# Optimization experiments

Hardware: AMD Instinct MI355X
Metric: run time of the kernel (lower is better)

## Reference

```python
import jax, jax.numpy as jnp
import numpy as np

NUM_HEADS = 16

def setup_inputs() -> dict:
    key = jax.random.key(0)
    ks = jax.random.split(key, 3)
    B, S, D = 2, 2048, 1024
    x = jax.random.normal(ks[0], (B, S, D), dtype=jnp.float32)
    # xavier-uniform style scaling for weights
    Wqkv = jax.random.normal(ks[1], (3 * D, D), dtype=jnp.float32) * (1.0 / jnp.sqrt(D))
    bqkv = jnp.zeros((3 * D,), dtype=jnp.float32)
    Wo = jax.random.normal(ks[2], (D, D), dtype=jnp.float32) * (1.0 / jnp.sqrt(D))
    bo = jnp.zeros((D,), dtype=jnp.float32)
    return {"x": x, "Wqkv": Wqkv, "bqkv": bqkv, "Wo": Wo, "bo": bo}

def reference(x, Wqkv, bqkv, Wo, bo):
    B, S, D = x.shape
    H = NUM_HEADS
    hd = D // H
    # qkv projection (torch Linear: x @ W.T + b)
    qkv = x @ Wqkv.T + bqkv                      # [B, S, 3D]
    qkv = qkv.reshape(B, S, H, 3 * hd).transpose(0, 2, 1, 3)  # [B, H, S, 3hd]
    q, k, v = jnp.split(qkv, 3, axis=-1)         # each [B, H, S, hd]
    scale = 1.0 / jnp.sqrt(jnp.asarray(hd, dtype=x.dtype))
    logits = jnp.einsum('bhqd,bhkd->bhqk', q, k) * scale  # [B, H, S, S]
    attn = jax.nn.softmax(logits, axis=-1)
    vals = jnp.einsum('bhqk,bhkd->bhqd', attn, v)         # [B, H, S, hd]
    vals = vals.transpose(0, 2, 1, 3).reshape(B, S, D)
    return vals @ Wo.T + bo
```

## Files before the change

kernel.cpp:

```cpp
#include <hip/hip_runtime.h>


typedef short short8 __attribute__((ext_vector_type(8)));
typedef unsigned short ushort8v __attribute__((ext_vector_type(8)));
typedef unsigned short ushort4v __attribute__((ext_vector_type(4)));
typedef float floatx4 __attribute__((ext_vector_type(4)));

#define S_LEN 2048
#define D_MODEL 1024
#define N_HEADS 16
#define HEAD_DIM 64

#define EXP2F(x) __builtin_amdgcn_exp2f(x)

__device__ inline float bf2f(unsigned int u16) {
    union { unsigned int i; float f; } v; v.i = u16 << 16; return v.f;
}
__device__ inline unsigned short f2b(float f) {
    union { float f; unsigned int u; } v; v.f = f;
    return (unsigned short)((v.u + 0x7FFFu + ((v.u >> 16) & 1u)) >> 16);
}
__device__ inline unsigned int fbits(float f) {
    union { float f; unsigned int u; } v; v.f = f; return v.u;
}
__device__ inline unsigned int pack_bf2(float lo, float hi) {
    return __byte_perm(fbits(lo) + 0x8000u, fbits(hi) + 0x8000u, 0x7632);
}

__device__ inline int key128(int c) {
    return (c & 0x63) | ((c & 0x0C) << 1) | ((c & 0x10) >> 2);
}

__device__ inline void gld_lds16(const unsigned short* g, unsigned short* lds) {
    __builtin_amdgcn_global_load_lds(
        (const __attribute__((address_space(1))) void*)g,
        (__attribute__((address_space(3))) void*)lds, 16, 0, 0);
}

__global__ __launch_bounds__(256)
void cvt3(const float* __restrict__ s0, const float* __restrict__ s1,
          const float* __restrict__ s2,
          unsigned short* __restrict__ d0, unsigned short* __restrict__ d1,
          unsigned short* __restrict__ d2,
          int n0, int n1, int n2) {
    const int total = n0 + n1 + n2;
    for (int g = blockIdx.x * blockDim.x + threadIdx.x; g < total;
         g += gridDim.x * blockDim.x) {
        const float* s; unsigned short* d; int l;
        if (g < n0)            { s = s0; d = d0; l = g; }
        else if (g < n0 + n1)  { s = s1; d = d1; l = g - n0; }
        else                   { s = s2; d = d2; l = g - n0 - n1; }
        const float4* sp = (const float4*)s + (size_t)l * 2;
        float4 f0 = sp[0], f1 = sp[1];
        ushort8v o;
        o[0] = f2b(f0.x); o[1] = f2b(f0.y); o[2] = f2b(f0.z); o[3] = f2b(f0.w);
        o[4] = f2b(f1.x); o[5] = f2b(f1.y); o[6] = f2b(f1.z); o[7] = f2b(f1.w);
        *(ushort8v*)(d + (size_t)l * 8) = o;
    }
}

__device__ inline void stage_u(const unsigned short* __restrict__ g, int ldk,
                               unsigned short* lds, int wave, int lane) {
    const int lr  = lane >> 3;
    const int csw = ((lane & 7) ^ lr) * 8;
    gld_lds16(g + (size_t)(wave * 8 + lr) * ldk + csw, lds + wave * 512);
}

#define STAGE_A(kk0, buf) do {                                                 \
    _Pragma("unroll")                                                          \
    for (int u = 0; u < 4; ++u)                                                \
        stage_u(Abase + (size_t)(u * 64) * K + (kk0), K,                       \
                &AS[buf][u * 4096], wave, lane);                               \
} while (0)
#define STAGE_B2(kk0, buf) do {                                 \
    stage_u(Bbase + (kk0),                    K, &BS[buf][0],    wave, lane);  \
    stage_u(Bbase + (size_t)64 * K + (kk0),   K, &BS[buf][4096], wave, lane);  \
} while (0)
#define STAGE_B1(kk0, buf) do {                                    \
    stage_u(Bbase + (size_t)128 * K + (kk0),  K, &BS[buf][8192], wave, lane);  \
} while (0)

#define QLDB(pBx) do {                                                         \
    _Pragma("unroll")                                                          \
    for (int nj = 0; nj < 3; ++nj) {                                           \
        bF[nj][0] = *(const short8*)((pBx) + nj * 1024 + co0);                 \
        bF[nj][1] = *(const short8*)((pBx) + nj * 1024 + co1);                 \
    }                                                                          \
} while (0)

#define QPHASE(pAx, mq, ...) do {                                              \
    short8 aF[2][2];                                                           \
    _Pragma("unroll")                                                          \
    for (int m2 = 0; m2 < 2; ++m2) {                                           \
        aF[m2][0] = *(const short8*)((pAx) + ((mq) * 2 + m2) * 1024 + co0);    \
        aF[m2][1] = *(const short8*)((pAx) + ((mq) * 2 + m2) * 1024 + co1);    \
    }                                                                          \
    __VA_ARGS__;                                                               \
    __builtin_amdgcn_s_barrier();                                              \
    __builtin_amdgcn_s_setprio(1);                                             \
    _Pragma("unroll")                                                          \
    for (int kk = 0; kk < 2; ++kk)                                             \
        _Pragma("unroll")                                                      \
        for (int m2 = 0; m2 < 2; ++m2)                                         \
            _Pragma("unroll")                                                  \
            for (int nj = 0; nj < 3; ++nj)                                     \
                acc[(mq) * 2 + m2][nj] = __builtin_amdgcn_mfma_f32_16x16x32_bf16( \
                    aF[m2][kk], bF[nj][kk], acc[(mq) * 2 + m2][nj], 0, 0, 0);  \
    __builtin_amdgcn_s_setprio(0);                                             \
    __builtin_amdgcn_s_barrier();                                              \
} while (0)

#define WAIT_VM3() asm volatile("s_waitcnt vmcnt(3)" ::: "memory")
#define WAIT_VM0() asm volatile("s_waitcnt vmcnt(0)" ::: "memory")

__global__ __launch_bounds__(512, 2)
void qkv_gemm(const unsigned short* __restrict__ x,
              const unsigned short* __restrict__ Wqkv,
              const float* __restrict__ bqkv,
              unsigned short* __restrict__ Qb,
              unsigned short* __restrict__ Kb,
              unsigned short* __restrict__ Vb) {
    __shared__ unsigned short AS[2][16384];
    __shared__ unsigned short BS[2][12288];

    const int tid  = threadIdx.x;
    const int lane = tid & 63;
    const int wave = tid >> 6;
    const int wm = wave >> 2;
    const int wn = wave & 3;
    const int r  = lane & 15, q2 = lane >> 4;
    const int K  = D_MODEL;

    const int idx = blockIdx.x;
    const int swz = (idx & 7) * 32 + (idx >> 3);
    const int mb = swz & 15, nb = swz >> 4;
    const int m0 = mb * 256, n0 = nb * 192;

    const unsigned short* Abase = x    + (size_t)m0 * K;
    const unsigned short* Bbase = Wqkv + (size_t)n0 * K;

    const int co0 = ((q2 ^ (r & 7)) * 8);
    const int co1 = (((q2 + 4) ^ (r & 7)) * 8);
    const unsigned short* pA0 = &AS[0][(wm * 128 + r) * 64];
    const unsigned short* pA1 = &AS[1][(wm * 128 + r) * 64];
    const unsigned short* pB0 = &BS[0][(wn * 48 + r) * 64];
    const unsigned short* pB1 = &BS[1][(wn * 48 + r) * 64];

    floatx4 acc[8][3] = {};
    short8 bF[3][2];

    STAGE_A(0, 0);
    STAGE_B2(0, 0); STAGE_B1(0, 0);
    STAGE_B2(64, 1); STAGE_B1(64, 1);
    WAIT_VM3();
    __builtin_amdgcn_s_barrier();

    for (int i = 0; i < 8; ++i) {
        const bool more = (i < 7);
        const int kA1 = i * 128 + 64;
        const int kT2 = i * 128 + 128;
        const int kT3 = i * 128 + 192;

        QLDB(pB0);
        QPHASE(pA0, 0, { STAGE_A(kA1, 1); });
        QPHASE(pA0, 1, { if (more) STAGE_B2(kT2, 0); });
        QPHASE(pA0, 2, { if (more) STAGE_B1(kT2, 0); });
        QPHASE(pA0, 3, {
            if (more) { WAIT_VM3(); } else { WAIT_VM0(); }
        });
        QLDB(pB1);
        QPHASE(pA1, 0, { if (more) STAGE_A(kT2, 0); });
        QPHASE(pA1, 1, { if (more) STAGE_B2(kT3, 1); });
        QPHASE(pA1, 2, { if (more) STAGE_B1(kT3, 1); });
        QPHASE(pA1, 3, {
            if (more) { WAIT_VM3(); }
        });
    }

#pragma unroll
    for (int mi = 0; mi < 8; mi++) {
#pragma unroll
        for (int nj = 0; nj < 3; nj++) {
            int rem = wn * 48 + nj * 16 + r;
            int n = n0 + rem;
            int typ = rem >> 6;
            int d = rem & 63;
            float bv = bqkv[n];
            int m = m0 + wm * 128 + mi * 16 + q2 * 4;
            int b = m >> 11, s = m & 2047;
            if (typ == 2) {
                ushort4v pk;
#pragma unroll
                for (int rg = 0; rg < 4; rg++) pk[rg] = f2b(acc[mi][nj][rg] + bv);
                *(ushort4v*)(Vb + ((size_t)((b * N_HEADS + nb) * HEAD_DIM + d)) * S_LEN + s) = pk;
            } else {
                unsigned short* dst = (typ == 0) ? Qb : Kb;
                float sc = (typ == 0) ? 0.180336880f : 1.0f;
#pragma unroll
                for (int rg = 0; rg < 4; rg++)
                    dst[(((size_t)(b * N_HEADS + nb)) * S_LEN + s + rg) * HEAD_DIM + d] =
                        f2b((acc[mi][nj][rg] + bv) * sc);
            }
        }
    }
}

__global__ __launch_bounds__(256)
void out_gemm(const unsigned short* __restrict__ vals,
              const unsigned short* __restrict__ Wo,
              const float* __restrict__ bo,
              float* __restrict__ out) {
    __shared__ unsigned short As[2][8192];
    __shared__ unsigned short Bs[2][4096];

    const int tid  = threadIdx.x;
    const int lane = tid & 63;
    const int wave = tid >> 6;
    const int wm = wave >> 1, wn = wave & 1;
    const int r = lane & 15, q2 = lane >> 4;
    const int K = D_MODEL;
    const int m0 = blockIdx.y * 128;
    const int n0 = blockIdx.x * 64;

    const unsigned short* Abase = vals + (size_t)m0 * K;
    const unsigned short* Bbase = Wo   + (size_t)n0 * K;

    const int lr  = lane >> 3;
    const int csw = ((lane & 7) ^ lr) * 8;
    const int co0 = ((q2 ^ (r & 7)) * 8);
    const int co1 = (((q2 + 4) ^ (r & 7)) * 8);

    floatx4 acc[4][2] = {};

#define OSTAGE(k0, abuf, bbuf) do {                                            \
    _Pragma("unroll")                                                          \
    for (int u = 0; u < 4; ++u)                                                \
        gld_lds16(Abase + (size_t)(u * 32 + wave * 8 + lr) * K + (k0) + csw,   \
                  (abuf) + u * 2048 + wave * 512);                             \
    _Pragma("unroll")                                                          \
    for (int u = 0; u < 2; ++u)                                                \
        gld_lds16(Bbase + (size_t)(u * 32 + wave * 8 + lr) * K + (k0) + csw,   \
                  (bbuf) + u * 2048 + wave * 512);                             \
} while (0)

    OSTAGE(0, &As[0][0], &Bs[0][0]);
    __builtin_amdgcn_s_waitcnt(0);
    __syncthreads();

    int buf = 0;
    for (int k0 = 0; k0 < K; k0 += 64) {
        const bool more = (k0 + 64 < K);
        if (more) {
            OSTAGE(k0 + 64, &As[buf ^ 1][0], &Bs[buf ^ 1][0]);
        }
#pragma unroll
        for (int kk = 0; kk < 2; kk++) {
            const int co = kk ? co1 : co0;
            short8 aF[4], bF[2];
#pragma unroll
            for (int t = 0; t < 4; t++)
                aF[t] = *(const short8*)(&As[buf][(wm * 64 + t * 16 + r) * 64] + co);
#pragma unroll
            for (int t = 0; t < 2; t++)
                bF[t] = *(const short8*)(&Bs[buf][(wn * 32 + t * 16 + r) * 64] + co);
#pragma unroll
            for (int i = 0; i < 4; i++)
#pragma unroll
                for (int j = 0; j < 2; j++)
                    acc[i][j] = __builtin_amdgcn_mfma_f32_16x16x32_bf16(aF[i], bF[j], acc[i][j], 0, 0, 0);
        }
        if (more) {
            __builtin_amdgcn_s_waitcnt(0);
            __syncthreads();
            buf ^= 1;
        }
    }
#undef OSTAGE

#pragma unroll
    for (int i = 0; i < 4; i++) {
#pragma unroll
        for (int j = 0; j < 2; j++) {
            int n = n0 + wn * 32 + j * 16 + r;
            float bv = bo[n];
#pragma unroll
            for (int rg = 0; rg < 4; rg++) {
                int m = m0 + wm * 64 + i * 16 + q2 * 4 + rg;
                out[(size_t)m * D_MODEL + n] = acc[i][j][rg] + bv;
            }
        }
    }
}

__global__ __launch_bounds__(256, 2)
void attn_kernel(const unsigned short* __restrict__ Qb,
                 const unsigned short* __restrict__ Kb,
                 const unsigned short* __restrict__ Vg,
                 unsigned short* __restrict__ vals) {
    __shared__ unsigned short Ks[2 * 128 * 64];
    __shared__ unsigned short Vts[2 * 128 * 64];

    const int tid = threadIdx.x;
    const int lane = tid & 63;
    const int wave = tid >> 6;
    const int r = lane & 15, q2 = lane >> 4;
    const int r7 = r & 7;
    const int w32 = wave * 32;

    const int idx  = blockIdx.x;
    const int xcd  = idx & 7;
    const int slot = idx >> 3;
    const int bh   = (xcd << 2) | (slot >> 4);
    const int q0   = (slot & 15) * 128;
    const int b = bh >> 4, h = bh & 15;

    const unsigned short* Qp = Qb + (size_t)bh * S_LEN * HEAD_DIM;
    const unsigned short* Kp = Kb + (size_t)bh * S_LEN * HEAD_DIM;
    const unsigned short* Vp = Vg + (size_t)bh * HEAD_DIM * S_LEN;

    const int srow = lane >> 3;
    const int scol = ((lane & 7) ^ srow) * 8;

    int krow[4], vd[4], vpan[4];
#pragma unroll
    for (int t = 0; t < 4; t++) {
        int c = wave * 32 + t * 8 + srow;
        krow[t] = key128(c);
        vpan[t] = c >> 6;
        vd[t]   = c & 63;
    }

    {
        const int qrow = tid >> 1;
        const int c0 = (tid & 1) * 4;
#pragma unroll
        for (int cc = 0; cc < 4; cc++) {
            int cb = c0 + cc;
            const uint4* gq = (const uint4*)(Qp + (size_t)(q0 + qrow) * HEAD_DIM + cb * 8);
            *(uint4*)(Ks + qrow * 64 + ((cb ^ (qrow & 7)) * 8)) = *gq;
        }
    }
    __syncthreads();
    short8 qf[2][2];
#pragma unroll
    for (int nt = 0; nt < 2; nt++)
#pragma unroll
        for (int ks = 0; ks < 2; ks++) {
            int cb = ks * 4 + q2;
            qf[nt][ks] = *(const short8*)(Ks + (w32 + nt * 16 + r) * 64 + ((cb ^ r7) * 8));
        }
    __syncthreads();

#pragma unroll
    for (int t = 0; t < 4; t++) {
        gld_lds16(Kp + (size_t)krow[t] * HEAD_DIM + scol,
                  Ks + (wave * 32 + t * 8) * 64);
        gld_lds16(Vp + (size_t)vd[t] * S_LEN + vpan[t] * 64 + scol,
                  Vts + (wave * 32 + t * 8) * 64);
    }
    __builtin_amdgcn_s_waitcnt(0);
    __syncthreads();

    union { unsigned int u[4]; short8 s; } onesu;
    onesu.u[0] = 0x3F803F80u; onesu.u[1] = 0x3F803F80u;
    onesu.u[2] = 0x3F803F80u; onesu.u[3] = 0x3F803F80u;
    const short8 onesf = onesu.s;

    floatx4 l_acc[2] = {};
    floatx4 o_acc[2][4] = {};
    int cur = 0;

    for (int kt = 0; kt < S_LEN; kt += 128) {
        const int more = (kt + 128 < S_LEN);
        if (more) {
            const int nxt = (cur ^ 1) * 8192;
#pragma unroll
            for (int t = 0; t < 4; t++) {
                gld_lds16(Kp + (size_t)(kt + 128 + krow[t]) * HEAD_DIM + scol,
                          Ks + nxt + (wave * 32 + t * 8) * 64);
                gld_lds16(Vp + (size_t)vd[t] * S_LEN + kt + 128 + vpan[t] * 64 + scol,
                          Vts + nxt + (wave * 32 + t * 8) * 64);
            }
        }
        const int co = cur * 8192;

        floatx4 sp[8][2] = {};
        __builtin_amdgcn_s_setprio(1);
#pragma unroll
        for (int mt = 0; mt < 8; mt++)
#pragma unroll
            for (int ks = 0; ks < 2; ks++) {
                int cb = ks * 4 + q2;
                short8 kfr = *(const short8*)(Ks + co + (mt * 16 + r) * 64 + ((cb ^ r7) * 8));
#pragma unroll
                for (int nt = 0; nt < 2; nt++)
                    sp[mt][nt] = __builtin_amdgcn_mfma_f32_16x16x32_bf16(kfr, qf[nt][ks], sp[mt][nt], 0, 0, 0);
            }
        __builtin_amdgcn_s_setprio(0);

#pragma unroll
        for (int nt = 0; nt < 2; nt++)
#pragma unroll
            for (int mt = 0; mt < 8; mt++)
#pragma unroll
                for (int reg = 0; reg < 4; reg++)
                    sp[mt][nt][reg] = EXP2F(sp[mt][nt][reg]);

        short8 pa[2][4];
#pragma unroll
        for (int nt = 0; nt < 2; nt++)
#pragma unroll
            for (int ks = 0; ks < 4; ks++) {
                union { unsigned int u[4]; short8 s; } tw;
                tw.u[0] = pack_bf2(sp[2 * ks][nt][0],     sp[2 * ks][nt][1]);
                tw.u[1] = pack_bf2(sp[2 * ks][nt][2],     sp[2 * ks][nt][3]);
                tw.u[2] = pack_bf2(sp[2 * ks + 1][nt][0], sp[2 * ks + 1][nt][1]);
                tw.u[3] = pack_bf2(sp[2 * ks + 1][nt][2], sp[2 * ks + 1][nt][3]);
                pa[nt][ks] = tw.s;
            }

        __builtin_amdgcn_s_setprio(1);
#pragma unroll
        for (int dt = 0; dt < 4; dt++) {
            short8 vf[4];
#pragma unroll
            for (int ks = 0; ks < 4; ks++) {
                int cb = (ks & 1) * 4 + q2;
                vf[ks] = *(const short8*)(Vts + co + (ks >> 1) * 4096 + (dt * 16 + r) * 64 + ((cb ^ r7) * 8));
            }
#pragma unroll
            for (int nt = 0; nt < 2; nt++)
#pragma unroll
                for (int ks = 0; ks < 4; ks++)
                    o_acc[nt][dt] = __builtin_amdgcn_mfma_f32_16x16x32_bf16(pa[nt][ks], vf[ks], o_acc[nt][dt], 0, 0, 0);
        }
#pragma unroll
        for (int nt = 0; nt < 2; nt++)
#pragma unroll
            for (int ks = 0; ks < 4; ks++)
                l_acc[nt] = __builtin_amdgcn_mfma_f32_16x16x32_bf16(pa[nt][ks], onesf, l_acc[nt], 0, 0, 0);
        __builtin_amdgcn_s_setprio(0);

        if (more) {
            __builtin_amdgcn_s_waitcnt(0);
            __syncthreads();
            cur ^= 1;
        }
    }

#pragma unroll
    for (int nt = 0; nt < 2; nt++) {
#pragma unroll
        for (int reg = 0; reg < 4; reg++) {
            float inv = 1.0f / l_acc[nt][reg];
            int srow2 = q0 + w32 + nt * 16 + q2 * 4 + reg;
            size_t base = ((size_t)b * S_LEN + srow2) * D_MODEL + h * HEAD_DIM + r;
#pragma unroll
            for (int dt = 0; dt < 4; dt++)
                vals[base + dt * 16] = f2b(o_acc[nt][dt][reg] * inv);
        }
    }
}

extern "C" void kernel_launch(void* const* d_in, const int* in_sizes, int n_in,
                              void* d_out, int out_size, void* d_ws, size_t ws_size,
                              hipStream_t stream) {
    const float* x    = (const float*)d_in[0];
    const float* Wqkv = (const float*)d_in[1];
    const float* bqkv = (const float*)d_in[2];
    const float* Wo   = (const float*)d_in[3];
    const float* bo   = (const float*)d_in[4];
    float* out = (float*)d_out;

    const size_t NX = 4194304, NW = 3145728, NO = 1048576;
    unsigned short* xb    = (unsigned short*)d_ws;
    unsigned short* Wqkvb = xb + NX;
    unsigned short* Wob   = Wqkvb + NW;
    unsigned short* Qb    = Wob + NO;
    unsigned short* Kb    = Qb + NX;
    unsigned short* Vb    = Kb + NX;
    unsigned short* vals  = xb;

    cvt3<<<4096, 256, 0, stream>>>(x, Wqkv, Wo, xb, Wqkvb, Wob,
                                   (int)(NX / 8), (int)(NW / 8), (int)(NO / 8));
    qkv_gemm<<<256, 512, 0, stream>>>(xb, Wqkvb, bqkv, Qb, Kb, Vb);
    attn_kernel<<<512, 256, 0, stream>>>(Qb, Kb, Vb, vals);
    out_gemm<<<dim3(16, 32), 256, 0, stream>>>(vals, Wob, bo, out);
}
```

Baseline: 174.4 us.

## Software-pipeline attention loop: overlap next QK^T with current PV, triple-buffer V

Restructures the attention inner loop so each iteration computes QK^T for tile t+1 while doing PV for tile t, with the exp/pack done after both. V moves to a three-slot LDS ring and two tiles are prefetched in the prologue, so loads run two tiles ahead. The aim is to hide exp latency and the load/barrier stalls behind MFMA work. The cost is more LDS (larger V buffer, possibly lower occupancy) and higher register pressure from keeping the packed probabilities live across the QK step.

```diff
diff --git a/kernel.cpp b/kernel.cpp
--- a/kernel.cpp
+++ b/kernel.cpp
@@ -298,7 +298,7 @@
                  const unsigned short* __restrict__ Vg,
                  unsigned short* __restrict__ vals) {
     __shared__ unsigned short Ks[2 * 128 * 64];
-    __shared__ unsigned short Vts[2 * 128 * 64];
+    __shared__ unsigned short V3[3 * 128 * 64];
 
     const int tid = threadIdx.x;
     const int lane = tid & 63;
@@ -356,9 +356,16 @@
         gld_lds16(Kp + (size_t)krow[t] * HEAD_DIM + scol,
                   Ks + (wave * 32 + t * 8) * 64);
         gld_lds16(Vp + (size_t)vd[t] * S_LEN + vpan[t] * 64 + scol,
-                  Vts + (wave * 32 + t * 8) * 64);
-    }
-    __builtin_amdgcn_s_waitcnt(0);
+                  V3 + (wave * 32 + t * 8) * 64);
+    }
+#pragma unroll
+    for (int t = 0; t < 4; t++) {
+        gld_lds16(Kp + (size_t)(128 + krow[t]) * HEAD_DIM + scol,
+                  Ks + 8192 + (wave * 32 + t * 8) * 64);
+        gld_lds16(Vp + (size_t)vd[t] * S_LEN + 128 + vpan[t] * 64 + scol,
+                  V3 + 8192 + (wave * 32 + t * 8) * 64);
+    }
+    asm volatile("s_waitcnt vmcnt(8)" ::: "memory");
     __syncthreads();
 
     union { unsigned int u[4]; short8 s; } onesu;
@@ -368,85 +375,112 @@
 
     floatx4 l_acc[2] = {};
     floatx4 o_acc[2][4] = {};
-    int cur = 0;
-
-    for (int kt = 0; kt < S_LEN; kt += 128) {
-        const int more = (kt + 128 < S_LEN);
-        if (more) {
-            const int nxt = (cur ^ 1) * 8192;
-#pragma unroll
-            for (int t = 0; t < 4; t++) {
-                gld_lds16(Kp + (size_t)(kt + 128 + krow[t]) * HEAD_DIM + scol,
-                          Ks + nxt + (wave * 32 + t * 8) * 64);
-                gld_lds16(Vp + (size_t)vd[t] * S_LEN + kt + 128 + vpan[t] * 64 + scol,
-                          Vts + nxt + (wave * 32 + t * 8) * 64);
+    floatx4 sp[8][2];
+    short8 paA[2][4];
+
+#define AZERO() do {                                                           \
+    _Pragma("unroll")                                                          \
+    for (int mt = 0; mt < 8; mt++)                                             \
+        _Pragma("unroll")                                                      \
+        for (int nt = 0; nt < 2; nt++)                                         \
+            sp[mt][nt] = (floatx4){0.f, 0.f, 0.f, 0.f};                        \
+} while (0)
+
+#define AQK(KBASE) do {                                                        \
+    _Pragma("unroll")                                                          \
+    for (int mt = 0; mt < 8; mt++)                                             \
+        _Pragma("unroll")                                                      \
+        for (int ks = 0; ks < 2; ks++) {                                       \
+            int cb = ks * 4 + q2;                                              \
+            short8 kfr = *(const short8*)(Ks + (KBASE) + (mt * 16 + r) * 64 + ((cb ^ r7) * 8)); \
+            _Pragma("unroll")                                                  \
+            for (int nt = 0; nt < 2; nt++)                                     \
+                sp[mt][nt] = __builtin_amdgcn_mfma_f32_16x16x32_bf16(kfr, qf[nt][ks], sp[mt][nt], 0, 0, 0); \
+        }                                                                      \
+} while (0)
+
+#define AEXPPACK() do {                                                        \
+    _Pragma("unroll")                                                          \
+    for (int nt = 0; nt < 2; nt++)                                             \
+        _Pragma("unroll")                                                      \
+        for (int mt = 0; mt < 8; mt++)                                         \
+            _Pragma("unroll")                                                  \
+            for (int reg = 0; reg < 4; reg++)                                  \
+                sp[mt][nt][reg] = EXP2F(sp[mt][nt][reg]);                      \
+    _Pragma("unroll")                                                          \
+    for (int nt = 0; nt < 2; nt++)                                             \
+        _Pragma("unroll")                                                      \
+        for (int ks = 0; ks < 4; ks++) {                                       \
+            union { unsigned int u[4]; short8 s; } tw;                         \
+            tw.u[0] = pack_bf2(sp[2 * ks][nt][0],     sp[2 * ks][nt][1]);      \
+            tw.u[1] = pack_bf2(sp[2 * ks][nt][2],     sp[2 * ks][nt][3]);      \
+            tw.u[2] = pack_bf2(sp[2 * ks + 1][nt][0], sp[2 * ks + 1][nt][1]);  \
+            tw.u[3] = pack_bf2(sp[2 * ks + 1][nt][2], sp[2 * ks + 1][nt][3]);  \
+            paA[nt][ks] = tw.s;                                                \
+        }                                                                      \
+} while (0)
+
+#define APVL(VBASE) do {                                                       \
+    _Pragma("unroll")                                                          \
+    for (int dt = 0; dt < 4; dt++) {                                           \
+        short8 vf[4];                                                          \
+        _Pragma("unroll")                                                      \
+        for (int ks = 0; ks < 4; ks++) {                                       \
+            int cb = (ks & 1) * 4 + q2;                                        \
+            vf[ks] = *(const short8*)(V3 + (VBASE) + (ks >> 1) * 4096 + (dt * 16 + r) * 64 + ((cb ^ r7) * 8)); \
+        }                                                                      \
+        _Pragma("unroll")                                                      \
+        for (int nt = 0; nt < 2; nt++)                                         \
+            _Pragma("unroll")                                                  \
+            for (int ks = 0; ks < 4; ks++)                                     \
+                o_acc[nt][dt] = __builtin_amdgcn_mfma_f32_16x16x32_bf16(paA[nt][ks], vf[ks], o_acc[nt][dt], 0, 0, 0); \
+    }                                                                          \
+    _Pragma("unroll")                                                          \
+    for (int nt = 0; nt < 2; nt++)                                             \
+        _Pragma("unroll")                                                      \
+        for (int ks = 0; ks < 4; ks++)                                         \
+            l_acc[nt] = __builtin_amdgcn_mfma_f32_16x16x32_bf16(paA[nt][ks], onesf, l_acc[nt], 0, 0, 0); \
+} while (0)
+
+    AZERO();
+    __builtin_amdgcn_s_setprio(1);
+    AQK(0);
+    __builtin_amdgcn_s_setprio(0);
+    AEXPPACK();
+
+    for (int t = 0; t < 15; ++t) {
+        asm volatile("s_waitcnt vmcnt(0)" ::: "memory");
+        __syncthreads();
+        if (t < 14) {
+            const int kb  = (t & 1) * 8192;
+            const int vs  = ((t + 2) % 3) * 8192;
+            const int kt2 = (t + 2) * 128;
+#pragma unroll
+            for (int tt = 0; tt < 4; tt++) {
+                gld_lds16(Kp + (size_t)(kt2 + krow[tt]) * HEAD_DIM + scol,
+                          Ks + kb + (wave * 32 + tt * 8) * 64);
+                gld_lds16(Vp + (size_t)vd[tt] * S_LEN + kt2 + vpan[tt] * 64 + scol,
+                          V3 + vs + (wave * 32 + tt * 8) * 64);
             }
         }
-        const int co = cur * 8192;
-
-        floatx4 sp[8][2] = {};
+        const int kc = ((t + 1) & 1) * 8192;
+        const int vb = (t % 3) * 8192;
+        AZERO();
         __builtin_amdgcn_s_setprio(1);
-#pragma unroll
-        for (int mt = 0; mt < 8; mt++)
-#pragma unroll
-            for (int ks = 0; ks < 2; ks++) {
-                int cb = ks * 4 + q2;
-                short8 kfr = *(const short8*)(Ks + co + (mt * 16 + r) * 64 + ((cb ^ r7) * 8));
-#pragma unroll
-                for (int nt = 0; nt < 2; nt++)
-                    sp[mt][nt] = __builtin_amdgcn_mfma_f32_16x16x32_bf16(kfr, qf[nt][ks], sp[mt][nt], 0, 0, 0);
-            }
+        AQK(kc);
+        APVL(vb);
         __builtin_amdgcn_s_setprio(0);
-
-#pragma unroll
-        for (int nt = 0; nt < 2; nt++)
-#pragma unroll
-            for (int mt = 0; mt < 8; mt++)
-#pragma unroll
-                for (int reg = 0; reg < 4; reg++)
-                    sp[mt][nt][reg] = EXP2F(sp[mt][nt][reg]);
-
-        short8 pa[2][4];
-#pragma unroll
-        for (int nt = 0; nt < 2; nt++)
-#pragma unroll
-            for (int ks = 0; ks < 4; ks++) {
-                union { unsigned int u[4]; short8 s; } tw;
-                tw.u[0] = pack_bf2(sp[2 * ks][nt][0],     sp[2 * ks][nt][1]);
-                tw.u[1] = pack_bf2(sp[2 * ks][nt][2],     sp[2 * ks][nt][3]);
-                tw.u[2] = pack_bf2(sp[2 * ks + 1][nt][0], sp[2 * ks + 1][nt][1]);
-                tw.u[3] = pack_bf2(sp[2 * ks + 1][nt][2], sp[2 * ks + 1][nt][3]);
-                pa[nt][ks] = tw.s;
-            }
-
-        __builtin_amdgcn_s_setprio(1);
-#pragma unroll
-        for (int dt = 0; dt < 4; dt++) {
-            short8 vf[4];
-#pragma unroll
-            for (int ks = 0; ks < 4; ks++) {
-                int cb = (ks & 1) * 4 + q2;
-                vf[ks] = *(const short8*)(Vts + co + (ks >> 1) * 4096 + (dt * 16 + r) * 64 + ((cb ^ r7) * 8));
-            }
-#pragma unroll
-            for (int nt = 0; nt < 2; nt++)
-#pragma unroll
-                for (int ks = 0; ks < 4; ks++)
-                    o_acc[nt][dt] = __builtin_amdgcn_mfma_f32_16x16x32_bf16(pa[nt][ks], vf[ks], o_acc[nt][dt], 0, 0, 0);
-        }
-#pragma unroll
-        for (int nt = 0; nt < 2; nt++)
-#pragma unroll
-            for (int ks = 0; ks < 4; ks++)
-                l_acc[nt] = __builtin_amdgcn_mfma_f32_16x16x32_bf16(pa[nt][ks], onesf, l_acc[nt], 0, 0, 0);
-        __builtin_amdgcn_s_setprio(0);
-
-        if (more) {
-            __builtin_amdgcn_s_waitcnt(0);
-            __syncthreads();
-            cur ^= 1;
-        }
-    }
+        AEXPPACK();
+    }
+
+    __builtin_amdgcn_s_setprio(1);
+    APVL(0);
+    __builtin_amdgcn_s_setprio(0);
+
+#undef AZERO
+#undef AQK
+#undef AEXPPACK
+#undef APVL
 
 #pragma unroll
     for (int nt = 0; nt < 2; nt++) {
```

Result: no change. 172.9 us (-0.8%).
